# Performance work log

Measured on AMD Instinct MI355X. Metric: run time of the kernel, lower is better.

The kernel has to match this reference:

```python
import jax, jax.numpy as jnp
import numpy as np

N = 50000          # nodes
E = 800000         # edges (avg degree 16)
D_IN = 128
D_HID = 128
D_OUT = 64
NUM_GRAPHS = 64


def setup_inputs() -> dict:
    key = jax.random.key(0)
    ks = jax.random.split(key, 10)
    x = jax.random.normal(ks[0], (N, D_IN), dtype=jnp.float32)
    edge_index = jax.random.randint(ks[1], (2, E), 0, N, dtype=jnp.int64)
    batch = jnp.sort(jax.random.randint(ks[2], (N,), 0, NUM_GRAPHS, dtype=jnp.int64))
    def glorot(k, fan_in, fan_out):
        s = np.float32(np.sqrt(6.0 / (fan_in + fan_out)))
        return jax.random.uniform(k, (fan_in, fan_out), jnp.float32, -s, s)
    return {
        "x": x,
        "edge_index": edge_index,
        "batch": batch,
        "W1": glorot(ks[3], D_IN, D_HID),  "b1": jnp.zeros((D_HID,), jnp.float32),
        "W2": glorot(ks[4], D_HID, D_HID), "b2": jnp.zeros((D_HID,), jnp.float32),
        "W3": glorot(ks[5], D_HID, D_OUT), "b3": jnp.zeros((D_OUT,), jnp.float32),
    }


def _gcn_conv(x, W, b, src, dst, dis):
    # GCNConv: D^{-1/2}(A+I)D^{-1/2} X W + b  (self-loops handled analytically)
    h = x @ W                                   # [N, out]
    norm = dis[src] * dis[dst]                  # [E]
    agg = jax.ops.segment_sum(h[src] * norm[:, None], dst, num_segments=N)
    return agg + h * (dis * dis)[:, None] + b   # self-loop term + bias


def reference(x, edge_index, batch, W1, b1, W2, b2, W3, b3):
    src, dst = edge_index[0], edge_index[1]
    # degree with self-loop (matches PyG add_self_loops + gcn_norm)
    deg = jnp.zeros((N,), jnp.float32).at[dst].add(1.0) + 1.0
    dis = jax.lax.rsqrt(deg)                    # deg >= 1, no inf handling needed

    h = jax.nn.relu(_gcn_conv(x, W1, b1, src, dst, dis))
    h = jax.nn.relu(_gcn_conv(h, W2, b2, src, dst, dis))
    features = _gcn_conv(h, W3, b3, src, dst, dis)   # [N, D_OUT]

    sums = jax.ops.segment_sum(features, batch, num_segments=NUM_GRAPHS)
    cnts = jax.ops.segment_sum(jnp.ones((N,), jnp.float32), batch, num_segments=NUM_GRAPHS)
    avg_pool = sums / jnp.maximum(cnts, 1.0)[:, None]  # [NUM_GRAPHS, D_OUT]
    return features, avg_pool
```

## Files before the change

kernel.cpp:

```cpp
#include <hip/hip_runtime.h>


constexpr int KDIM = 128;
constexpr int NGRAPH = 64;

__global__ void k_init(int* __restrict__ counts, int n) {
  int i = blockIdx.x * blockDim.x + threadIdx.x;
  int stride = gridDim.x * blockDim.x;
  for (int j = i; j < n; j += stride) counts[j] = 0;
}

__global__ void k_hist(const int* __restrict__ src, const int* __restrict__ dst,
                       int* __restrict__ counts, int e, int n) {
  int i = blockIdx.x * blockDim.x + threadIdx.x;
  int stride = gridDim.x * blockDim.x;
  for (int j = i; j < e; j += stride) {
    int s = src[j], d = dst[j];
    if ((unsigned)s < (unsigned)n && (unsigned)d < (unsigned)n)
      atomicAdd(&counts[d], 1);
  }
}

__global__ void k_dis(const int* __restrict__ counts, float* __restrict__ dis, int n) {
  int i = blockIdx.x * blockDim.x + threadIdx.x;
  int stride = gridDim.x * blockDim.x;
  for (int j = i; j < n; j += stride)
    dis[j] = rsqrtf((float)counts[j] + 1.0f);
}

__global__ void k_scan_block(const int* __restrict__ in, int* __restrict__ outExcl,
                             int* __restrict__ blockSums, int n) {
  __shared__ int s[256];
  int tid = threadIdx.x;
  int i = blockIdx.x * 256 + tid;
  int v = (i < n) ? in[i] : 0;
  int x = v;
  s[tid] = x;
  __syncthreads();
  for (int off = 1; off < 256; off <<= 1) {
    int t = (tid >= off) ? s[tid - off] : 0;
    __syncthreads();
    x += t;
    s[tid] = x;
    __syncthreads();
  }
  if (i < n) outExcl[i] = x - v;
  if (tid == 255) blockSums[blockIdx.x] = x;
}

__global__ void k_scan_offsets(int* __restrict__ bs, int nb) {
  __shared__ int s[256];
  int tid = threadIdx.x;
  int v = (tid < nb) ? bs[tid] : 0;
  int x = v;
  s[tid] = x;
  __syncthreads();
  for (int off = 1; off < 256; off <<= 1) {
    int t = (tid >= off) ? s[tid - off] : 0;
    __syncthreads();
    x += t;
    s[tid] = x;
    __syncthreads();
  }
  if (tid < nb) bs[tid] = x - v;
  if (tid == nb - 1) bs[256] = x;
}

__global__ void k_scan_add(int* __restrict__ row_start, const int* __restrict__ bs,
                           int* __restrict__ cursor, int n) {
  int i = blockIdx.x * blockDim.x + threadIdx.x;
  int stride = gridDim.x * blockDim.x;
  for (int j = i; j < n; j += stride) {
    int r = row_start[j] + bs[j >> 8];
    row_start[j] = r;
    cursor[j] = r;
  }
  if (i == 0) row_start[n] = bs[256];
}

__global__ void k_scatter(const int* __restrict__ src, const int* __restrict__ dst,
                          int* __restrict__ cursor, int* __restrict__ colA,
                          int e, int n) {
  int i = blockIdx.x * blockDim.x + threadIdx.x;
  int stride = gridDim.x * blockDim.x;
  for (int j = i; j < e; j += stride) {
    int s = src[j], d = dst[j];
    if ((unsigned)s < (unsigned)n && (unsigned)d < (unsigned)n) {
      int pos = atomicAdd(&cursor[d], 1);
      colA[pos] = s;
    }
  }
}

template <int DOUT>
__global__ __launch_bounds__(256) void k_gemm2(const float* __restrict__ X,
                                               const float* __restrict__ W,
                                               float* __restrict__ H, int n) {
  __shared__ float xT[32][128];
  __shared__ float Wl[32][64];
  const int tid = threadIdx.x;
  const int tr = tid & 15;
  const int tc = tid >> 4;
  const int rowBase = blockIdx.x * 128;
  const int colBase = blockIdx.y * 64;

  float acc[8][4];
#pragma unroll
  for (int i = 0; i < 8; ++i)
#pragma unroll
    for (int j = 0; j < 4; ++j) acc[i][j] = 0.f;

  const int sr = tid >> 1;
  const int kh = (tid & 1) * 16;
  const int srow = min(rowBase + sr, n - 1);
  const float* xsrc = X + (size_t)srow * KDIM + kh;

  for (int k0 = 0; k0 < KDIM / 32; ++k0) {
    {
      const float4* s4 = reinterpret_cast<const float4*>(xsrc + k0 * 32);
      float4 v0 = s4[0], v1 = s4[1], v2 = s4[2], v3 = s4[3];
      xT[kh + 0][sr] = v0.x;  xT[kh + 1][sr] = v0.y;
      xT[kh + 2][sr] = v0.z;  xT[kh + 3][sr] = v0.w;
      xT[kh + 4][sr] = v1.x;  xT[kh + 5][sr] = v1.y;
      xT[kh + 6][sr] = v1.z;  xT[kh + 7][sr] = v1.w;
      xT[kh + 8][sr] = v2.x;  xT[kh + 9][sr] = v2.y;
      xT[kh + 10][sr] = v2.z; xT[kh + 11][sr] = v2.w;
      xT[kh + 12][sr] = v3.x; xT[kh + 13][sr] = v3.y;
      xT[kh + 14][sr] = v3.z; xT[kh + 15][sr] = v3.w;
    }
#pragma unroll
    for (int q = 0; q < 2; ++q) {
      int f4 = tid + q * 256;
      int k = f4 >> 4;
      int c4 = f4 & 15;
      *reinterpret_cast<float4*>(&Wl[k][c4 * 4]) = *reinterpret_cast<const float4*>(
          W + (size_t)(k0 * 32 + k) * DOUT + colBase + c4 * 4);
    }
    __syncthreads();
#pragma unroll 8
    for (int k = 0; k < 32; ++k) {
      float4 xa = *reinterpret_cast<const float4*>(&xT[k][tr * 4]);
      float4 xb = *reinterpret_cast<const float4*>(&xT[k][64 + tr * 4]);
      float4 wv = *reinterpret_cast<const float4*>(&Wl[k][tc * 4]);
      const float xs[8] = {xa.x, xa.y, xa.z, xa.w, xb.x, xb.y, xb.z, xb.w};
      const float ws[4] = {wv.x, wv.y, wv.z, wv.w};
#pragma unroll
      for (int i = 0; i < 8; ++i)
#pragma unroll
        for (int j = 0; j < 4; ++j) acc[i][j] = fmaf(xs[i], ws[j], acc[i][j]);
    }
    __syncthreads();
  }

#pragma unroll
  for (int i = 0; i < 8; ++i) {
    int row = rowBase + ((i < 4) ? (tr * 4 + i) : (64 + tr * 4 + i - 4));
    if (row < n) {
      float4 o = {acc[i][0], acc[i][1], acc[i][2], acc[i][3]};
      *reinterpret_cast<float4*>(H + (size_t)row * DOUT + colBase + tc * 4) = o;
    }
  }
}

template <int D, bool RELU>
__global__ __launch_bounds__(256) void k_agg2(const float* __restrict__ H,
                                              const int* __restrict__ row_start,
                                              const int* __restrict__ colA,
                                              const float* __restrict__ dis,
                                              const float* __restrict__ bias,
                                              float* __restrict__ OUT, int n) {
  const int wave = threadIdx.x >> 6;
  const int lane = threadIdx.x & 63;
  const int slot = wave >> 1;
  const int half = wave & 1;
  const int node = blockIdx.x * 2 + slot;
  constexpr int C = D / 64;
  __shared__ float red[4][D];

  if (node < n) {
    const int beg = row_start[node];
    const int end = row_start[node + 1];
    const float di = dis[node];
    float accA[C], accB[C];
#pragma unroll
    for (int c = 0; c < C; ++c) { accA[c] = 0.f; accB[c] = 0.f; }
    int e = beg + half;
    for (; e + 2 < end; e += 4) {
      const int s0 = colA[e], s1 = colA[e + 2];
      const float n0 = dis[s0] * di, n1 = dis[s1] * di;
      const float* h0 = H + (size_t)s0 * D;
      const float* h1 = H + (size_t)s1 * D;
#pragma unroll
      for (int c = 0; c < C; ++c) {
        accA[c] = fmaf(h0[lane + 64 * c], n0, accA[c]);
        accB[c] = fmaf(h1[lane + 64 * c], n1, accB[c]);
      }
    }
    for (; e < end; e += 2) {
      const int s0 = colA[e];
      const float n0 = dis[s0] * di;
      const float* h0 = H + (size_t)s0 * D;
#pragma unroll
      for (int c = 0; c < C; ++c) accA[c] = fmaf(h0[lane + 64 * c], n0, accA[c]);
    }
#pragma unroll
    for (int c = 0; c < C; ++c) red[wave][lane + 64 * c] = accA[c] + accB[c];
  } else {
#pragma unroll
    for (int c = 0; c < C; ++c) red[wave][lane + 64 * c] = 0.f;
  }
  __syncthreads();
  if (half == 0 && node < n) {
    const float di = dis[node];
    const float di2 = di * di;
    const float* hn = H + (size_t)node * D;
    float* o = OUT + (size_t)node * D;
#pragma unroll
    for (int c = 0; c < C; ++c) {
      float v = red[wave][lane + 64 * c] + red[wave + 1][lane + 64 * c] +
                hn[lane + 64 * c] * di2 + bias[lane + 64 * c];
      if (RELU) v = fmaxf(v, 0.f);
      o[lane + 64 * c] = v;
    }
  }
}

__global__ __launch_bounds__(256) void k_pool2(const float* __restrict__ F,
                                               const int* __restrict__ batch,
                                               float* __restrict__ out, int n) {
  const int g = blockIdx.x;
  __shared__ int sb[2];
  if (threadIdx.x < 2) {
    int target = g + threadIdx.x;
    int lo = 0, hi = n;
    while (lo < hi) {
      int mid = (lo + hi) >> 1;
      if (batch[mid] < target) lo = mid + 1; else hi = mid;
    }
    sb[threadIdx.x] = lo;
  }
  __syncthreads();
  const int beg = sb[0], end = sb[1];
  const int wave = threadIdx.x >> 6;
  const int lane = threadIdx.x & 63;
  float acc = 0.f;
  for (int node = beg + wave; node < end; node += 4)
    acc += F[(size_t)node * 64 + lane];
  __shared__ float red[4][64];
  red[wave][lane] = acc;
  __syncthreads();
  if (wave == 0) {
    float v = (red[0][lane] + red[1][lane]) + (red[2][lane] + red[3][lane]);
    out[g * 64 + lane] = v / fmaxf((float)(end - beg), 1.f);
  }
}

extern "C" void kernel_launch(void* const* d_in, const int* in_sizes, int n_in,
                              void* d_out, int out_size, void* d_ws, size_t ws_size,
                              hipStream_t stream) {
  const float* x     = (const float*)d_in[0];
  const int*   ei    = (const int*)d_in[1];
  const int*   batch = (const int*)d_in[2];
  const float* W1 = (const float*)d_in[3];
  const float* b1 = (const float*)d_in[4];
  const float* W2 = (const float*)d_in[5];
  const float* b2 = (const float*)d_in[6];
  const float* W3 = (const float*)d_in[7];
  const float* b3 = (const float*)d_in[8];

  const int n = in_sizes[0] / KDIM;
  const int e = in_sizes[1] / 2;
  const int* src = ei;
  const int* dst = ei + e;

  char* p = (char*)d_ws;
  size_t off = 0;
  auto carve = [&](size_t bytes) {
    char* r = p + off;
    off = (off + bytes + 255) & ~(size_t)255;
    return r;
  };
  float* bufA      = (float*)carve((size_t)n * KDIM * 4);
  float* bufB      = (float*)carve((size_t)n * KDIM * 4);
  float* dis       = (float*)carve((size_t)n * 4);
  int*   counts    = (int*)carve((size_t)n * 4);
  int*   row_start = (int*)carve((size_t)(n + 1) * 4);
  int*   cursor    = (int*)carve((size_t)n * 4);
  int*   colA      = (int*)carve((size_t)e * 4);
  int*   blockSums = (int*)carve(512 * 4);
  (void)ws_size;

  const int nb1 = (n + 255) / 256;
  const int GS = 1024;

  k_init<<<GS, 256, 0, stream>>>(counts, n);
  k_hist<<<GS, 256, 0, stream>>>(src, dst, counts, e, n);
  k_dis<<<nb1, 256, 0, stream>>>(counts, dis, n);
  k_scan_block<<<nb1, 256, 0, stream>>>(counts, row_start, blockSums, n);
  k_scan_offsets<<<1, 256, 0, stream>>>(blockSums, nb1);
  k_scan_add<<<nb1, 256, 0, stream>>>(row_start, blockSums, cursor, n);
  k_scatter<<<GS, 256, 0, stream>>>(src, dst, cursor, colA, e, n);

  const int rowBlocks = (n + 127) / 128;
  const int aggGrid = (n + 1) / 2;

  k_gemm2<128><<<dim3(rowBlocks, 2), 256, 0, stream>>>(x, W1, bufA, n);
  k_agg2<128, true><<<aggGrid, 256, 0, stream>>>(bufA, row_start, colA, dis, b1, bufB, n);
  k_gemm2<128><<<dim3(rowBlocks, 2), 256, 0, stream>>>(bufB, W2, bufA, n);
  k_agg2<128, true><<<aggGrid, 256, 0, stream>>>(bufA, row_start, colA, dis, b2, bufB, n);
  k_gemm2<64><<<dim3(rowBlocks, 1), 256, 0, stream>>>(bufB, W3, bufA, n);
  k_agg2<64, false><<<aggGrid, 256, 0, stream>>>(bufA, row_start, colA, dis, b3,
                                                 (float*)d_out, n);
  k_pool2<<<NGRAPH, 256, 0, stream>>>((const float*)d_out, batch,
                                      (float*)d_out + (size_t)n * 64, n);
}
```

Measured before the change: 523.4 us.

## Split aggregation into 16-feature column slices across interleaved blocks

The gather-aggregation kernel now gives each wave one node and one 16-wide feature slice. Four lanes groups process four edges in parallel, and the partial sums are reduced with cross-lane shuffles instead of shared memory and a block barrier. Consecutive blocks cover different slices of the same nodes, which is meant to give more parallelism and keep neighbour rows in L2 across slices. In exchange, each gather now reads only 64-byte segments, and every slice re-reads the edge indices and degree factors. Edge index loads use nontemporal hints.

```diff
diff --git a/kernel.cpp b/kernel.cpp
--- a/kernel.cpp
+++ b/kernel.cpp
@@ -163,65 +163,56 @@
 }
 
 template <int D, bool RELU>
-__global__ __launch_bounds__(256) void k_agg2(const float* __restrict__ H,
+__global__ __launch_bounds__(256) void k_agg5(const float* __restrict__ H,
                                               const int* __restrict__ row_start,
                                               const int* __restrict__ colA,
                                               const float* __restrict__ dis,
                                               const float* __restrict__ bias,
                                               float* __restrict__ OUT, int n) {
+  constexpr int NS = D / 16;
+  constexpr int NPG = 4 * (8 / NS);
+  const int r = blockIdx.x & 7;
+  const int nb = blockIdx.x >> 3;
+  const int slice = r % NS;
+  const int nodeSub = r / NS;
   const int wave = threadIdx.x >> 6;
   const int lane = threadIdx.x & 63;
-  const int slot = wave >> 1;
-  const int half = wave & 1;
-  const int node = blockIdx.x * 2 + slot;
-  constexpr int C = D / 64;
-  __shared__ float red[4][D];
-
-  if (node < n) {
-    const int beg = row_start[node];
-    const int end = row_start[node + 1];
-    const float di = dis[node];
-    float accA[C], accB[C];
-#pragma unroll
-    for (int c = 0; c < C; ++c) { accA[c] = 0.f; accB[c] = 0.f; }
-    int e = beg + half;
-    for (; e + 2 < end; e += 4) {
-      const int s0 = colA[e], s1 = colA[e + 2];
-      const float n0 = dis[s0] * di, n1 = dis[s1] * di;
-      const float* h0 = H + (size_t)s0 * D;
-      const float* h1 = H + (size_t)s1 * D;
-#pragma unroll
-      for (int c = 0; c < C; ++c) {
-        accA[c] = fmaf(h0[lane + 64 * c], n0, accA[c]);
-        accB[c] = fmaf(h1[lane + 64 * c], n1, accB[c]);
-      }
-    }
-    for (; e < end; e += 2) {
-      const int s0 = colA[e];
-      const float n0 = dis[s0] * di;
-      const float* h0 = H + (size_t)s0 * D;
-#pragma unroll
-      for (int c = 0; c < C; ++c) accA[c] = fmaf(h0[lane + 64 * c], n0, accA[c]);
-    }
-#pragma unroll
-    for (int c = 0; c < C; ++c) red[wave][lane + 64 * c] = accA[c] + accB[c];
-  } else {
-#pragma unroll
-    for (int c = 0; c < C; ++c) red[wave][lane + 64 * c] = 0.f;
-  }
-  __syncthreads();
-  if (half == 0 && node < n) {
-    const float di = dis[node];
+  const int esub = lane >> 4;
+  const int d = lane & 15;
+  const int node = nb * NPG + nodeSub * 4 + wave;
+  if (node >= n) return;
+
+  const int d0 = slice * 16;
+  const int beg = row_start[node];
+  const int end = row_start[node + 1];
+  const float di = dis[node];
+  float acc = 0.f;
+
+  int e = beg + esub;
+  for (; e + 4 < end; e += 8) {
+    const int s0 = __builtin_nontemporal_load(&colA[e]);
+    const int s1 = __builtin_nontemporal_load(&colA[e + 4]);
+    const float w0 = dis[s0] * di;
+    const float w1 = dis[s1] * di;
+    const float h0 = H[(size_t)s0 * D + d0 + d];
+    const float h1 = H[(size_t)s1 * D + d0 + d];
+    acc = fmaf(h0, w0, acc);
+    acc = fmaf(h1, w1, acc);
+  }
+  for (; e < end; e += 4) {
+    const int s0 = __builtin_nontemporal_load(&colA[e]);
+    const float w0 = dis[s0] * di;
+    acc = fmaf(H[(size_t)s0 * D + d0 + d], w0, acc);
+  }
+
+  acc += __shfl_xor(acc, 16);
+  acc += __shfl_xor(acc, 32);
+
+  if (esub == 0) {
     const float di2 = di * di;
-    const float* hn = H + (size_t)node * D;
-    float* o = OUT + (size_t)node * D;
-#pragma unroll
-    for (int c = 0; c < C; ++c) {
-      float v = red[wave][lane + 64 * c] + red[wave + 1][lane + 64 * c] +
-                hn[lane + 64 * c] * di2 + bias[lane + 64 * c];
-      if (RELU) v = fmaxf(v, 0.f);
-      o[lane + 64 * c] = v;
-    }
+    float v = acc + H[(size_t)node * D + d0 + d] * di2 + bias[d0 + d];
+    if (RELU) v = fmaxf(v, 0.f);
+    OUT[(size_t)node * D + d0 + d] = v;
   }
 }
 
@@ -302,15 +293,16 @@
   k_scatter<<<GS, 256, 0, stream>>>(src, dst, cursor, colA, e, n);
 
   const int rowBlocks = (n + 127) / 128;
-  const int aggGrid = (n + 1) / 2;
+  const int aggGrid128 = 8 * ((n + 3) / 4);
+  const int aggGrid64  = 8 * ((n + 7) / 8);
 
   k_gemm2<128><<<dim3(rowBlocks, 2), 256, 0, stream>>>(x, W1, bufA, n);
-  k_agg2<128, true><<<aggGrid, 256, 0, stream>>>(bufA, row_start, colA, dis, b1, bufB, n);
+  k_agg5<128, true><<<aggGrid128, 256, 0, stream>>>(bufA, row_start, colA, dis, b1, bufB, n);
   k_gemm2<128><<<dim3(rowBlocks, 2), 256, 0, stream>>>(bufB, W2, bufA, n);
-  k_agg2<128, true><<<aggGrid, 256, 0, stream>>>(bufA, row_start, colA, dis, b2, bufB, n);
+  k_agg5<128, true><<<aggGrid128, 256, 0, stream>>>(bufA, row_start, colA, dis, b2, bufB, n);
   k_gemm2<64><<<dim3(rowBlocks, 1), 256, 0, stream>>>(bufB, W3, bufA, n);
-  k_agg2<64, false><<<aggGrid, 256, 0, stream>>>(bufA, row_start, colA, dis, b3,
-                                                 (float*)d_out, n);
+  k_agg5<64, false><<<aggGrid64, 256, 0, stream>>>(bufA, row_start, colA, dis, b3,
+                                                   (float*)d_out, n);
   k_pool2<<<NGRAPH, 256, 0, stream>>>((const float*)d_out, batch,
                                       (float*)d_out + (size_t)n * 64, n);
 }
```

Measured after the change: 829.7 us. 58.5% more time.
